# Kernel tuning notes

Hardware: AMD Instinct MI355X
Metric: run time of the kernel (lower is better)

Reference implementation:

```python
import jax, jax.numpy as jnp
import numpy as np
from jax import lax

VOCAB = 32000
EMBED = 300
HIDDEN = 1024
BATCH = 64
SEQLEN = 512


def setup_inputs() -> dict:
    key = jax.random.key(0)
    k1, k2, k3, k4 = jax.random.split(key, 4)
    seq = jax.random.randint(k1, (BATCH, SEQLEN), 0, VOCAB, dtype=jnp.int32)
    embedding_table = jax.random.normal(k2, (VOCAB, EMBED), dtype=jnp.float32) * 0.1
    # Keras LSTM params: kernel [E, 4H], recurrent_kernel [H, 4H], bias [4H]; gate order i,f,c,o
    kernel = jax.random.normal(k3, (EMBED, 4 * HIDDEN), dtype=jnp.float32) * (1.0 / np.sqrt(EMBED))
    recurrent_kernel = jax.random.normal(k4, (HIDDEN, 4 * HIDDEN), dtype=jnp.float32) * (1.0 / np.sqrt(HIDDEN))
    # Keras unit_forget_bias default: forget-gate bias = 1
    bias = jnp.concatenate([
        jnp.zeros((HIDDEN,), jnp.float32),
        jnp.ones((HIDDEN,), jnp.float32),
        jnp.zeros((2 * HIDDEN,), jnp.float32),
    ])
    return {"embedding_table": embedding_table, "kernel": kernel,
            "recurrent_kernel": recurrent_kernel, "bias": bias, "seq": seq}


def _masked_lstm(x, mask, kernel, recurrent_kernel, bias):
    # x: [B,T,E], mask: [B,T] bool. Returns final hidden state [B,H].
    B = x.shape[0]
    H = recurrent_kernel.shape[0]
    # precompute input projections for all steps: [T,B,4H]
    xz = jnp.einsum('bte,eg->tbg', x, kernel) + bias
    mask_t = mask.T  # [T,B]

    def step(carry, inp):
        h, c = carry
        zx, mt = inp  # zx [B,4H], mt [B]
        z = zx + h @ recurrent_kernel
        zi, zf, zg, zo = jnp.split(z, 4, axis=-1)
        i = jax.nn.sigmoid(zi)
        f = jax.nn.sigmoid(zf)
        g = jnp.tanh(zg)
        o = jax.nn.sigmoid(zo)
        c_new = f * c + i * g
        h_new = o * jnp.tanh(c_new)
        m = mt[:, None]
        h = jnp.where(m, h_new, h)
        c = jnp.where(m, c_new, c)
        return (h, c), None

    h0 = jnp.zeros((B, H), x.dtype)
    c0 = jnp.zeros((B, H), x.dtype)
    (h, _), _ = lax.scan(step, (h0, c0), (xz, mask_t))
    return h


def reference(embedding_table, kernel, recurrent_kernel, bias, seq):
    x = embedding_table[seq]          # [B,T,E] embedding lookup
    mask = seq != 0                   # mask_zero=True: token id 0 is padding
    return _masked_lstm(x, mask, kernel, recurrent_kernel, bias)
```

## Files before the change

kernel.cpp:

```cpp
#include <hip/hip_runtime.h>

#define TT 512
#define BB 64
#define EE 300
#define HH 1024
#define GG 4096
#define NSLOT 33

typedef _Float16 f16x8 __attribute__((ext_vector_type(8)));
typedef float f32x4 __attribute__((ext_vector_type(4)));


__device__ __forceinline__ float sigmf(float x) {
    return __fdividef(1.0f, 1.0f + __expf(-x));
}
__device__ __forceinline__ float tanhsf(float x) {
    float e = __expf(-2.0f * fabsf(x));
    float r = __fdividef(1.0f - e, 1.0f + e);
    return copysignf(r, x);
}

__global__ void mask_kernel(const int* __restrict__ seq, float* __restrict__ maskf) {
    int idx = blockIdx.x * 256 + threadIdx.x;
    int t = idx >> 6, b = idx & 63;
    maskf[idx] = (seq[b * TT + t] != 0) ? 1.0f : 0.0f;
}

__global__ __launch_bounds__(256)
void xgather_kernel(const float* __restrict__ emb, const int* __restrict__ seq,
                    _Float16* __restrict__ xA) {
    __shared__ float xrow[64 * 305];
    const int t = blockIdx.x, tid = threadIdx.x;
    const int r = tid >> 2, sub = tid & 3;
    const int row = seq[r * TT + t];
    for (int e = sub; e < EE; e += 4)
        xrow[r * 305 + e] = emb[row * EE + e];
    __syncthreads();
    unsigned int* dst = (unsigned int*)(xA + (size_t)t * 20480);
    for (int idx = tid; idx < 10240; idx += 256) {
        int el = idx << 1;
        int j = el & 7, b = (el >> 3) & 63, quad = (el >> 9) & 3, kb = el >> 11;
        int e = (kb << 5) + (quad << 3) + j;
        union { _Float16 h[2]; unsigned int u; } pk;
        pk.h[0] = (e < EE)     ? (_Float16)xrow[b * 305 + e]     : (_Float16)0.f;
        pk.h[1] = (e + 1 < EE) ? (_Float16)xrow[b * 305 + e + 1] : (_Float16)0.f;
        dst[idx] = pk.u;
    }
}

__global__ __launch_bounds__(512, 2)
void lstm_kernel(const _Float16* __restrict__ xA, const float* __restrict__ rk,
                 const float* __restrict__ wk, const float* __restrict__ bias,
                 const float* __restrict__ maskf, _Float16* __restrict__ hbuf,
                 unsigned int* __restrict__ flags, float* __restrict__ out) {
    __shared__ _Float16 RbL[16384];
    __shared__ _Float16 WbL[5120];
    __shared__ float zb[8704];
    __shared__ float cs[2048];
    __shared__ _Float16 hshh[256];
    const int tid = threadIdx.x;
    const int lane = tid & 63;
    const int w = tid >> 6;
    const int p = blockIdx.x;
    const int p4 = p << 2;
    const int cc = lane & 15, quad = lane >> 4;

    for (int i = tid; i < 16384; i += 512) {
        int k = i >> 4, c = i & 15;
        float v = rk[k * GG + ((c >> 2) << 10) + p4 + (c & 3)];
        RbL[((k >> 5) << 9) + (((k >> 3) & 3) << 7) + (c << 3) + (k & 7)] = (_Float16)v;
    }
    for (int i = tid; i < 5120; i += 512) {
        int e = i >> 4, c = i & 15;
        float v = (e < EE) ? wk[e * GG + ((c >> 2) << 10) + p4 + (c & 3)] : 0.f;
        WbL[((e >> 5) << 9) + (((e >> 3) & 3) << 7) + (c << 3) + (e & 7)] = (_Float16)v;
    }
    if (tid < 256) cs[tid] = 0.f;
    float bb[4];
    if (w < 4) {
#pragma unroll
        for (int gt = 0; gt < 4; ++gt)
            bb[gt] = bias[(gt << 10) + p4 + w];
    }
    int slot = 0, nslot = 1;
    float hown = 0.0f;
    const int fidx = (w << 5) + (lane & 31);
    const f16x8* RbH = (const f16x8*)RbL;
    const f16x8* WbH = (const f16x8*)WbL;
    __syncthreads();

    for (int t = 0; t < TT; ++t) {
        float m = maskf[(t << 6) + lane];
        f32x4 acc[4];
#pragma unroll
        for (int mt = 0; mt < 4; ++mt) acc[mt] = (f32x4){0.f, 0.f, 0.f, 0.f};

        const f16x8* xA8 = (const f16x8*)(xA + (size_t)t * 20480);
        {
            int kb = w;
            f16x8 bf = WbH[(kb << 6) + (quad << 4) + cc];
#pragma unroll
            for (int mt = 0; mt < 4; ++mt) {
                f16x8 af = xA8[(kb << 8) + (quad << 6) + (mt << 4) + cc];
                acc[mt] = __builtin_amdgcn_mfma_f32_16x16x32_f16(af, bf, acc[mt], 0, 0, 0);
            }
        }
        if (w < 2) {
            int kb = 8 + w;
            f16x8 bf = WbH[(kb << 6) + (quad << 4) + cc];
#pragma unroll
            for (int mt = 0; mt < 4; ++mt) {
                f16x8 af = xA8[(kb << 8) + (quad << 6) + (mt << 4) + cc];
                acc[mt] = __builtin_amdgcn_mfma_f32_16x16x32_f16(af, bf, acc[mt], 0, 0, 0);
            }
        }

        if (t > 0) {
            unsigned int tgt = (unsigned int)t;
            while (!__all((int)(__hip_atomic_load(flags + fidx, __ATOMIC_RELAXED,
                                                  __HIP_MEMORY_SCOPE_AGENT) >= tgt)))
                __builtin_amdgcn_s_sleep(1);
        }
        __builtin_amdgcn_sched_barrier(0);

        const f16x8* hA8 = (const f16x8*)(hbuf + (size_t)slot * 65536);
#pragma unroll
        for (int kc = 0; kc < 4; ++kc) {
            int kb = (w << 2) + kc;
            f16x8 bf = RbH[(kb << 6) + (quad << 4) + cc];
#pragma unroll
            for (int mt = 0; mt < 4; ++mt) {
                f16x8 af = hA8[(kb << 8) + (quad << 6) + (mt << 4) + cc];
                acc[mt] = __builtin_amdgcn_mfma_f32_16x16x32_f16(af, bf, acc[mt], 0, 0, 0);
            }
        }
#pragma unroll
        for (int mt = 0; mt < 4; ++mt)
            *(f32x4*)(zb + ((w << 4) + cc) * 68 + (mt << 4) + (quad << 2)) = acc[mt];
        __syncthreads();
        if (w < 4) {
            float z[4];
#pragma unroll
            for (int gt = 0; gt < 4; ++gt) {
                int c = (gt << 2) + w;
                float s = bb[gt];
#pragma unroll
                for (int wp = 0; wp < 8; ++wp) s += zb[((wp << 4) + c) * 68 + lane];
                z[gt] = s;
            }
            float fi = sigmf(z[0]);
            float ff = sigmf(z[1]);
            float fg = tanhsf(z[2]);
            float fo = sigmf(z[3]);
            float co = cs[(w << 6) + lane];
            float cn = fmaf(ff, co, fi * fg);
            cn = fmaf(m, cn - co, co);
            cs[(w << 6) + lane] = cn;
            float hc = fo * tanhsf(cn);
            hown = fmaf(m, hc - hown, hown);
            hshh[(lane << 2) + w] = (_Float16)hown;
        }
        __syncthreads();
        if (tid < 64) {
            unsigned long long hv = ((const unsigned long long*)hshh)[lane];
            size_t el = (size_t)nslot * 65536 + ((size_t)(p >> 3) << 11) +
                        ((size_t)((p >> 1) & 3) << 9) + (lane << 3) + ((p & 1) << 2);
            __hip_atomic_store((unsigned long long*)(hbuf + el), hv,
                               __ATOMIC_RELAXED, __HIP_MEMORY_SCOPE_AGENT);
        }
        __syncthreads();
        if (tid == 0)
            __hip_atomic_store(flags + p, (unsigned int)(t + 1),
                               __ATOMIC_RELAXED, __HIP_MEMORY_SCOPE_AGENT);
        slot = nslot;
        nslot = (nslot + 1 == NSLOT) ? 0 : nslot + 1;
    }
    if (w < 4) zb[(w << 6) + lane] = hown;
    __syncthreads();
    if (tid < 64) {
        float4 v = make_float4(zb[tid], zb[64 + tid], zb[128 + tid], zb[192 + tid]);
        *(float4*)(out + tid * HH + p4) = v;
    }
}

extern "C" void kernel_launch(void* const* d_in, const int* in_sizes, int n_in,
                              void* d_out, int out_size, void* d_ws, size_t ws_size,
                              hipStream_t stream) {
    const float* emb  = (const float*)d_in[0];
    const float* wk   = (const float*)d_in[1];
    const float* rk   = (const float*)d_in[2];
    const float* bias = (const float*)d_in[3];
    const int*   seq  = (const int*)d_in[4];
    float* out = (float*)d_out;
    char* ws = (char*)d_ws;

    const size_t off_hbuf = 1024;
    const size_t off_mask = off_hbuf + (size_t)NSLOT * 131072;
    const size_t off_xA   = off_mask + 131072;
    unsigned int* flags = (unsigned int*)ws;
    _Float16* hbuf  = (_Float16*)(ws + off_hbuf);
    float*    maskf = (float*)(ws + off_mask);
    _Float16* xA    = (_Float16*)(ws + off_xA);

    hipMemsetAsync(ws, 0, off_hbuf + 131072, stream);
    mask_kernel<<<128, 256, 0, stream>>>(seq, maskf);
    xgather_kernel<<<TT, 256, 0, stream>>>(emb, seq, xA);
    lstm_kernel<<<256, 512, 0, stream>>>(xA, rk, wk, bias, maskf, hbuf, flags, out);
}
```

Before: 1.891 ms.

## Prefetch next-step input projection off critical path and keep weight fragments in registers

Hoists the recurrent and input weight MFMA fragments from LDS into registers once before the time loop. Computes the next step's x·W contribution early: warps 4-6 do it during the gate phase, warp 7 does it after publishing h, and warps 0-3 do it after the gates. The separate barrier before the flag store is replaced by an explicit vmcnt wait in warp 7. The aim is to shorten the per-step serial chain of the recurrence, at the cost of higher register pressure and reliance on the waitcnt for ordering.

```diff
diff --git a/kernel.cpp b/kernel.cpp
--- a/kernel.cpp
+++ b/kernel.cpp
@@ -82,38 +82,43 @@
         for (int gt = 0; gt < 4; ++gt)
             bb[gt] = bias[(gt << 10) + p4 + w];
     }
-    int slot = 0, nslot = 1;
-    float hown = 0.0f;
     const int fidx = (w << 5) + (lane & 31);
     const f16x8* RbH = (const f16x8*)RbL;
     const f16x8* WbH = (const f16x8*)WbL;
     __syncthreads();
 
+    f16x8 Rreg[4];
+#pragma unroll
+    for (int kc = 0; kc < 4; ++kc)
+        Rreg[kc] = RbH[((((w << 2) + kc)) << 6) + (quad << 4) + cc];
+    f16x8 Wreg0 = WbH[(w << 6) + (quad << 4) + cc];
+    f16x8 Wreg1 = {};
+    if (w < 2) Wreg1 = WbH[((8 + w) << 6) + (quad << 4) + cc];
+
+    f32x4 acc[4];
+    auto XW = [&](int tt) {
+        const f16x8* xA8 = (const f16x8*)(xA + (size_t)tt * 20480);
+#pragma unroll
+        for (int mt = 0; mt < 4; ++mt) {
+            f16x8 af = xA8[(w << 8) + (quad << 6) + (mt << 4) + cc];
+            acc[mt] = __builtin_amdgcn_mfma_f32_16x16x32_f16(
+                af, Wreg0, (f32x4){0.f, 0.f, 0.f, 0.f}, 0, 0, 0);
+        }
+        if (w < 2) {
+#pragma unroll
+            for (int mt = 0; mt < 4; ++mt) {
+                f16x8 af = xA8[((8 + w) << 8) + (quad << 6) + (mt << 4) + cc];
+                acc[mt] = __builtin_amdgcn_mfma_f32_16x16x32_f16(af, Wreg1, acc[mt], 0, 0, 0);
+            }
+        }
+    };
+
+    XW(0);
+    int slot = 0, nslot = 1;
+    float hown = 0.0f;
+
     for (int t = 0; t < TT; ++t) {
-        float m = maskf[(t << 6) + lane];
-        f32x4 acc[4];
-#pragma unroll
-        for (int mt = 0; mt < 4; ++mt) acc[mt] = (f32x4){0.f, 0.f, 0.f, 0.f};
-
-        const f16x8* xA8 = (const f16x8*)(xA + (size_t)t * 20480);
-        {
-            int kb = w;
-            f16x8 bf = WbH[(kb << 6) + (quad << 4) + cc];
-#pragma unroll
-            for (int mt = 0; mt < 4; ++mt) {
-                f16x8 af = xA8[(kb << 8) + (quad << 6) + (mt << 4) + cc];
-                acc[mt] = __builtin_amdgcn_mfma_f32_16x16x32_f16(af, bf, acc[mt], 0, 0, 0);
-            }
-        }
-        if (w < 2) {
-            int kb = 8 + w;
-            f16x8 bf = WbH[(kb << 6) + (quad << 4) + cc];
-#pragma unroll
-            for (int mt = 0; mt < 4; ++mt) {
-                f16x8 af = xA8[(kb << 8) + (quad << 6) + (mt << 4) + cc];
-                acc[mt] = __builtin_amdgcn_mfma_f32_16x16x32_f16(af, bf, acc[mt], 0, 0, 0);
-            }
-        }
+        float m = (w < 4) ? maskf[(t << 6) + lane] : 0.f;
 
         if (t > 0) {
             unsigned int tgt = (unsigned int)t;
@@ -127,18 +132,21 @@
 #pragma unroll
         for (int kc = 0; kc < 4; ++kc) {
             int kb = (w << 2) + kc;
-            f16x8 bf = RbH[(kb << 6) + (quad << 4) + cc];
 #pragma unroll
             for (int mt = 0; mt < 4; ++mt) {
                 f16x8 af = hA8[(kb << 8) + (quad << 6) + (mt << 4) + cc];
-                acc[mt] = __builtin_amdgcn_mfma_f32_16x16x32_f16(af, bf, acc[mt], 0, 0, 0);
+                acc[mt] = __builtin_amdgcn_mfma_f32_16x16x32_f16(af, Rreg[kc], acc[mt], 0, 0, 0);
             }
         }
 #pragma unroll
         for (int mt = 0; mt < 4; ++mt)
             *(f32x4*)(zb + ((w << 4) + cc) * 68 + (mt << 4) + (quad << 2)) = acc[mt];
         __syncthreads();
-        if (w < 4) {
+
+        const bool more = (t + 1 < TT);
+        if (w >= 4) {
+            if (w != 7 && more) XW(t + 1);
+        } else {
             float z[4];
 #pragma unroll
             for (int gt = 0; gt < 4; ++gt) {
@@ -161,17 +169,20 @@
             hshh[(lane << 2) + w] = (_Float16)hown;
         }
         __syncthreads();
-        if (tid < 64) {
+
+        if (w == 7) {
             unsigned long long hv = ((const unsigned long long*)hshh)[lane];
             size_t el = (size_t)nslot * 65536 + ((size_t)(p >> 3) << 11) +
                         ((size_t)((p >> 1) & 3) << 9) + (lane << 3) + ((p & 1) << 2);
             __hip_atomic_store((unsigned long long*)(hbuf + el), hv,
                                __ATOMIC_RELAXED, __HIP_MEMORY_SCOPE_AGENT);
-        }
-        __syncthreads();
-        if (tid == 0)
-            __hip_atomic_store(flags + p, (unsigned int)(t + 1),
-                               __ATOMIC_RELAXED, __HIP_MEMORY_SCOPE_AGENT);
+            asm volatile("s_waitcnt vmcnt(0)" ::: "memory");
+            if (lane == 0)
+                __hip_atomic_store(flags + p, (unsigned int)(t + 1),
+                                   __ATOMIC_RELAXED, __HIP_MEMORY_SCOPE_AGENT);
+            if (more) XW(t + 1);
+        }
+        if (w < 4 && more) XW(t + 1);
         slot = nslot;
         nslot = (nslot + 1 == NSLOT) ? 0 : nslot + 1;
     }
```

Result: slower. 3.651 ms (+93.0%).
